# Kernel optimization log

Measured on AMD Instinct MI355X. Metric: run time of the kernel, lower is better.

## Reference

```python
import jax, jax.numpy as jnp
import numpy as np


def setup_inputs() -> dict:
    key = jax.random.key(0)
    k1, k2 = jax.random.split(key)
    B, N, M, D = 4, 8192, 8192, 3
    pred = jax.random.normal(k1, (B, N, D), dtype=jnp.float32)
    target = jax.random.normal(k2, (B, M, D), dtype=jnp.float32)
    return {"pred": pred, "target": target}


def reference(pred, target):
    # Pairwise squared distances via the GEMM cross-term trick:
    # ||p - t||^2 = ||p||^2 + ||t||^2 - 2 <p, t>
    pn = jnp.sum(pred * pred, axis=-1)            # [B, N]
    tn = jnp.sum(target * target, axis=-1)        # [B, M]
    cross = jnp.einsum('bnd,bmd->bnm', pred, target)  # [B, N, M]
    dist = pn[:, :, None] + tn[:, None, :] - 2.0 * cross
    d_pt = jnp.min(dist, axis=2)  # [B, N] pred -> nearest target
    d_tp = jnp.min(dist, axis=1)  # [B, M] target -> nearest pred
    return jnp.mean(d_pt) + jnp.mean(d_tp)
```

## Files before the change

kernel.cpp:

```cpp
#include <hip/hip_runtime.h>
#include <hip/hip_bf16.h>


typedef __attribute__((ext_vector_type(8)))  short short8;
typedef __attribute__((ext_vector_type(16))) float f32x16;

#define BATCH 4
#define NPTS 8192
#define TOTALQ (BATCH * NPTS)
#define BLK 256
#define WNT 2
#define BROWS 256
#define NCH (TOTALQ / BROWS)
#define MSPLIT 8
#define MRANGE (NPTS / MSPLIT)
#define MT_PER (MRANGE / 32)
#define ROW_US 16

#define PACK_US ((size_t)TOTALQ * ROW_US)
#define PART_OFF ((size_t)4 * PACK_US * 2)

__device__ __forceinline__ unsigned short f2bf(float f) {
    unsigned int u = __float_as_uint(f);
    u += 0x7FFFu + ((u >> 16) & 1u);
    return (unsigned short)(u >> 16);
}
__device__ __forceinline__ float bf2f(unsigned short h) {
    return __uint_as_float(((unsigned int)h) << 16);
}
__device__ __forceinline__ unsigned int pk2(unsigned short a, unsigned short b) {
    return (unsigned int)a | ((unsigned int)b << 16);
}

__global__ __launch_bounds__(BLK) void chamfer_pack_kernel(
        const float* __restrict__ pred, const float* __restrict__ target,
        ushort* __restrict__ ws, float* __restrict__ out)
{
    int i = blockIdx.x * BLK + threadIdx.x;
    if (i == 0) out[0] = 0.0f;
    int which = i >> 15;
    int p = i & (TOTALQ - 1);
    const float* src = which ? target : pred;
    float x = src[3 * p], y = src[3 * p + 1], z = src[3 * p + 2];

    unsigned short hx = f2bf(x), hy = f2bf(y), hz = f2bf(z);
    unsigned short lx = f2bf(x - bf2f(hx)), ly = f2bf(y - bf2f(hy)),
                   lz = f2bf(z - bf2f(hz));
    float nrm = fmaf(z, z, fmaf(y, y, x * x));
    unsigned short n1 = f2bf(nrm);
    float r1 = nrm - bf2f(n1);
    unsigned short n2 = f2bf(r1);
    unsigned short n3 = f2bf(r1 - bf2f(n2));
    const unsigned short ONE = 0x3F80;

    unsigned short ax = f2bf(-2.f * bf2f(hx)), ay = f2bf(-2.f * bf2f(hy)),
                   az = f2bf(-2.f * bf2f(hz));
    unsigned short cx = f2bf(-2.f * bf2f(lx)), cy = f2bf(-2.f * bf2f(ly)),
                   cz = f2bf(-2.f * bf2f(lz));

    uint4 A0 = { pk2(ax, ay), pk2(az, cx), pk2(cy, cz), pk2(ax, ay) };
    uint4 A1 = { pk2(az, n1), pk2(n2, n3), pk2(ONE, ONE), pk2(ONE, 0) };
    uint4 B0 = { pk2(hx, hy), pk2(hz, hx), pk2(hy, hz), pk2(lx, ly) };
    uint4 B1 = { pk2(lz, ONE), pk2(ONE, ONE), pk2(n1, n2), pk2(n3, 0) };

    uint4* dA = (uint4*)(ws + (size_t)(2 * which) * PACK_US + (size_t)p * ROW_US);
    uint4* dB = (uint4*)(ws + (size_t)(2 * which + 1) * PACK_US + (size_t)p * ROW_US);
    dA[0] = A0;  dA[1] = A1;
    dB[0] = B0;  dB[1] = B1;
}

__global__ __launch_bounds__(BLK) void chamfer_mfma_kernel(
        const ushort* __restrict__ ws, float* __restrict__ part)
{
    const int dir = blockIdx.z;
    const ushort* packA = ws + (dir ? 2 * PACK_US : 0);
    const ushort* packB = ws + (dir ? 1 * PACK_US : 3 * PACK_US);

    const int nch = blockIdx.x;
    const int b   = nch >> 5;
    const int ms  = blockIdx.y;
    const int w    = threadIdx.x >> 6;
    const int lane = threadIdx.x & 63;
    const int c = lane & 31;
    const int g = lane >> 5;

    __shared__ uint4 ldsb[2][MRANGE];

    {
        const uint4* gB = (const uint4*)(packB +
            ((size_t)b * NPTS + (size_t)ms * MRANGE) * ROW_US);
        #pragma unroll
        for (int r = threadIdx.x; r < MRANGE; r += BLK) {
            ldsb[0][r] = gB[2 * r];
            ldsb[1][r] = gB[2 * r + 1];
        }
    }

    const int rowstart = nch * BROWS + w * (WNT * 32);
    short8 afrag[WNT];
    #pragma unroll
    for (int nt = 0; nt < WNT; ++nt) {
        afrag[nt] = *(const short8*)(
            packA + (size_t)(rowstart + nt * 32 + c) * ROW_US + 8 * g);
    }

    f32x16 acc[WNT];
    #pragma unroll
    for (int nt = 0; nt < WNT; ++nt)
        #pragma unroll
        for (int r = 0; r < 16; ++r)
            acc[nt][r] = 3.4e38f;
    const f32x16 zacc = (f32x16)(0.f);

    __syncthreads();

    const ushort* ldsu = (const ushort*)ldsb;

    #pragma unroll 4
    for (int mt = 0; mt < MT_PER; mt += 2) {
        short8 bf0 = *(const short8*)(ldsu + g * (MRANGE * 8) + (mt * 32 + c) * 8);
        short8 bf1 = *(const short8*)(ldsu + g * (MRANGE * 8) + ((mt + 1) * 32 + c) * 8);
        #pragma unroll
        for (int nt = 0; nt < WNT; ++nt) {
            f32x16 d0 = __builtin_amdgcn_mfma_f32_32x32x16_bf16(
                            afrag[nt], bf0, zacc, 0, 0, 0);
            f32x16 d1 = __builtin_amdgcn_mfma_f32_32x32x16_bf16(
                            afrag[nt], bf1, zacc, 0, 0, 0);
            #pragma unroll
            for (int r = 0; r < 16; ++r)
                acc[nt][r] = fminf(fminf(acc[nt][r], d0[r]), d1[r]);
        }
    }

    float* rp = part + (size_t)(dir * MSPLIT + ms) * TOTALQ + rowstart;
    #pragma unroll
    for (int nt = 0; nt < WNT; ++nt) {
        f32x16 v = acc[nt];
        #pragma unroll
        for (int m = 1; m < 32; m <<= 1) {
            #pragma unroll
            for (int r = 0; r < 16; ++r)
                v[r] = fminf(v[r], __shfl_xor(v[r], m, 64));
        }
        #pragma unroll
        for (int r = 0; r < 16; ++r) {
            int row = (r & 3) + 8 * (r >> 2) + 4 * g;
            if (c == r) rp[nt * 32 + row] = v[r];
        }
    }
}

__global__ __launch_bounds__(BLK) void chamfer_reduce_kernel(
        const float* __restrict__ part, float* __restrict__ out)
{
    int gl = blockIdx.x * BLK + threadIdx.x;
    int dir = gl >> 15, i = gl & (TOTALQ - 1);

    const float* p = part + (size_t)dir * MSPLIT * TOTALQ + i;
    float m = p[0];
    #pragma unroll
    for (int s = 1; s < MSPLIT; ++s)
        m = fminf(m, p[(size_t)s * TOTALQ]);

    float acc = m * (1.0f / (float)TOTALQ);
    #pragma unroll
    for (int off = 32; off > 0; off >>= 1)
        acc += __shfl_down(acc, off, 64);
    __shared__ float wsum[BLK / 64];
    int lane = threadIdx.x & 63, wid = threadIdx.x >> 6;
    if (lane == 0) wsum[wid] = acc;
    __syncthreads();
    if (threadIdx.x == 0) {
        float s = 0.0f;
        #pragma unroll
        for (int wv = 0; wv < BLK / 64; ++wv) s += wsum[wv];
        atomicAdd(out, s);
    }
}

extern "C" void kernel_launch(void* const* d_in, const int* in_sizes, int n_in,
                              void* d_out, int out_size, void* d_ws, size_t ws_size,
                              hipStream_t stream) {
    const float* pred   = (const float*)d_in[0];
    const float* target = (const float*)d_in[1];
    float*       out    = (float*)d_out;
    ushort*      wsp    = (ushort*)d_ws;
    float*       part   = (float*)((char*)d_ws + PART_OFF);

    hipLaunchKernelGGL(chamfer_pack_kernel, dim3(2 * TOTALQ / BLK), dim3(BLK),
                       0, stream, pred, target, wsp, out);

    dim3 grid(NCH, MSPLIT, 2);
    hipLaunchKernelGGL(chamfer_mfma_kernel, grid, dim3(BLK), 0, stream,
                       (const ushort*)wsp, part);

    hipLaunchKernelGGL(chamfer_reduce_kernel, dim3(2 * TOTALQ / BLK), dim3(BLK),
                       0, stream, (const float*)part, out);
}
```

Measured before the change: 95.58 us.

## Fuse point packing into MFMA kernel with staged LDS tiles and single-block reduce

Removes the separate pack kernel: each block now converts its query points and streams target points into LDS in 1024-point stages, splitting them into bf16 hi/lo/norm payloads on the fly. Block rows drop to 128 with one tile per wave and the column split drops to 2, so fewer partial minima are written. The final reduction becomes a single 1024-thread block writing the output directly, with no atomic. The trade-off is redundant per-block recomputation of target payloads, less A-tile reuse per LDS read, and a serial single-block reduce.

```diff
diff --git a/kernel.cpp b/kernel.cpp
--- a/kernel.cpp
+++ b/kernel.cpp
@@ -9,16 +9,13 @@
 #define NPTS 8192
 #define TOTALQ (BATCH * NPTS)
 #define BLK 256
-#define WNT 2
-#define BROWS 256
+#define BROWS 128
 #define NCH (TOTALQ / BROWS)
-#define MSPLIT 8
+#define MSPLIT 2
 #define MRANGE (NPTS / MSPLIT)
-#define MT_PER (MRANGE / 32)
-#define ROW_US 16
-
-#define PACK_US ((size_t)TOTALQ * ROW_US)
-#define PART_OFF ((size_t)4 * PACK_US * 2)
+#define MC 1024
+#define NSTAGE (MRANGE / MC)
+#define MT_PER (MC / 32)
 
 __device__ __forceinline__ unsigned short f2bf(float f) {
     unsigned int u = __float_as_uint(f);
@@ -32,149 +29,135 @@
     return (unsigned int)a | ((unsigned int)b << 16);
 }
 
-__global__ __launch_bounds__(BLK) void chamfer_pack_kernel(
-        const float* __restrict__ pred, const float* __restrict__ target,
-        ushort* __restrict__ ws, float* __restrict__ out)
-{
-    int i = blockIdx.x * BLK + threadIdx.x;
-    if (i == 0) out[0] = 0.0f;
-    int which = i >> 15;
-    int p = i & (TOTALQ - 1);
-    const float* src = which ? target : pred;
-    float x = src[3 * p], y = src[3 * p + 1], z = src[3 * p + 2];
-
-    unsigned short hx = f2bf(x), hy = f2bf(y), hz = f2bf(z);
-    unsigned short lx = f2bf(x - bf2f(hx)), ly = f2bf(y - bf2f(hy)),
-                   lz = f2bf(z - bf2f(hz));
+struct Payload {
+    unsigned short hx, hy, hz, lx, ly, lz, n1, n2, n3;
+};
+__device__ __forceinline__ Payload split_point(float x, float y, float z) {
+    Payload P;
+    P.hx = f2bf(x);  P.hy = f2bf(y);  P.hz = f2bf(z);
+    P.lx = f2bf(x - bf2f(P.hx));
+    P.ly = f2bf(y - bf2f(P.hy));
+    P.lz = f2bf(z - bf2f(P.hz));
     float nrm = fmaf(z, z, fmaf(y, y, x * x));
-    unsigned short n1 = f2bf(nrm);
-    float r1 = nrm - bf2f(n1);
-    unsigned short n2 = f2bf(r1);
-    unsigned short n3 = f2bf(r1 - bf2f(n2));
-    const unsigned short ONE = 0x3F80;
-
-    unsigned short ax = f2bf(-2.f * bf2f(hx)), ay = f2bf(-2.f * bf2f(hy)),
-                   az = f2bf(-2.f * bf2f(hz));
-    unsigned short cx = f2bf(-2.f * bf2f(lx)), cy = f2bf(-2.f * bf2f(ly)),
-                   cz = f2bf(-2.f * bf2f(lz));
-
-    uint4 A0 = { pk2(ax, ay), pk2(az, cx), pk2(cy, cz), pk2(ax, ay) };
-    uint4 A1 = { pk2(az, n1), pk2(n2, n3), pk2(ONE, ONE), pk2(ONE, 0) };
-    uint4 B0 = { pk2(hx, hy), pk2(hz, hx), pk2(hy, hz), pk2(lx, ly) };
-    uint4 B1 = { pk2(lz, ONE), pk2(ONE, ONE), pk2(n1, n2), pk2(n3, 0) };
-
-    uint4* dA = (uint4*)(ws + (size_t)(2 * which) * PACK_US + (size_t)p * ROW_US);
-    uint4* dB = (uint4*)(ws + (size_t)(2 * which + 1) * PACK_US + (size_t)p * ROW_US);
-    dA[0] = A0;  dA[1] = A1;
-    dB[0] = B0;  dB[1] = B1;
+    P.n1 = f2bf(nrm);
+    float r1 = nrm - bf2f(P.n1);
+    P.n2 = f2bf(r1);
+    P.n3 = f2bf(r1 - bf2f(P.n2));
+    return P;
 }
 
-__global__ __launch_bounds__(BLK) void chamfer_mfma_kernel(
-        const ushort* __restrict__ ws, float* __restrict__ part)
+__global__ __launch_bounds__(BLK) void chamfer_mega_kernel(
+        const float* __restrict__ pred, const float* __restrict__ target,
+        float* __restrict__ part)
 {
     const int dir = blockIdx.z;
-    const ushort* packA = ws + (dir ? 2 * PACK_US : 0);
-    const ushort* packB = ws + (dir ? 1 * PACK_US : 3 * PACK_US);
+    const float* __restrict__ Q  = dir ? target : pred;
+    const float* __restrict__ Tg = dir ? pred : target;
 
     const int nch = blockIdx.x;
-    const int b   = nch >> 5;
+    const int b   = nch >> 6;
     const int ms  = blockIdx.y;
     const int w    = threadIdx.x >> 6;
     const int lane = threadIdx.x & 63;
     const int c = lane & 31;
     const int g = lane >> 5;
+    const unsigned short ONE = 0x3F80;
 
-    __shared__ uint4 ldsb[2][MRANGE];
+    __shared__ uint4 ldsb[2][MC];
 
+    const int rowstart = nch * BROWS + w * 32;
+    short8 afrag;
     {
-        const uint4* gB = (const uint4*)(packB +
-            ((size_t)b * NPTS + (size_t)ms * MRANGE) * ROW_US);
+        int r = rowstart + c;
+        float x = Q[3 * r], y = Q[3 * r + 1], z = Q[3 * r + 2];
+        Payload P = split_point(x, y, z);
+        unsigned short ax = f2bf(-2.f * bf2f(P.hx)),
+                       ay = f2bf(-2.f * bf2f(P.hy)),
+                       az = f2bf(-2.f * bf2f(P.hz));
+        unsigned short cx = f2bf(-2.f * bf2f(P.lx)),
+                       cy = f2bf(-2.f * bf2f(P.ly)),
+                       cz = f2bf(-2.f * bf2f(P.lz));
+        uint4 h0 = { pk2(ax, ay), pk2(az, cx), pk2(cy, cz), pk2(ax, ay) };
+        uint4 h1 = { pk2(az, P.n1), pk2(P.n2, P.n3), pk2(ONE, ONE), pk2(ONE, 0) };
+        uint4 sel = g ? h1 : h0;
+        afrag = *(short8*)&sel;
+    }
+
+    f32x16 acc;
+    #pragma unroll
+    for (int r = 0; r < 16; ++r) acc[r] = 3.4e38f;
+    const f32x16 zacc = (f32x16)(0.f);
+
+    const size_t colbase = (size_t)b * NPTS + (size_t)ms * MRANGE;
+
+    for (int st = 0; st < NSTAGE; ++st) {
+        __syncthreads();
         #pragma unroll
-        for (int r = threadIdx.x; r < MRANGE; r += BLK) {
-            ldsb[0][r] = gB[2 * r];
-            ldsb[1][r] = gB[2 * r + 1];
+        for (int j = 0; j < MC / BLK; ++j) {
+            int p = j * BLK + threadIdx.x;
+            size_t gp = colbase + st * MC + p;
+            float x = Tg[3 * gp], y = Tg[3 * gp + 1], z = Tg[3 * gp + 2];
+            Payload P = split_point(x, y, z);
+            ldsb[0][p] = (uint4){ pk2(P.hx, P.hy), pk2(P.hz, P.hx),
+                                  pk2(P.hy, P.hz), pk2(P.lx, P.ly) };
+            ldsb[1][p] = (uint4){ pk2(P.lz, ONE), pk2(ONE, ONE),
+                                  pk2(P.n1, P.n2), pk2(P.n3, 0) };
+        }
+        __syncthreads();
+
+        const ushort* ldsu = (const ushort*)&ldsb[g][0];
+        #pragma unroll 2
+        for (int mt = 0; mt < MT_PER; mt += 2) {
+            short8 bf0 = *(const short8*)(ldsu + (mt * 32 + c) * 8);
+            short8 bf1 = *(const short8*)(ldsu + ((mt + 1) * 32 + c) * 8);
+            f32x16 d0 = __builtin_amdgcn_mfma_f32_32x32x16_bf16(
+                            afrag, bf0, zacc, 0, 0, 0);
+            f32x16 d1 = __builtin_amdgcn_mfma_f32_32x32x16_bf16(
+                            afrag, bf1, zacc, 0, 0, 0);
+            #pragma unroll
+            for (int r = 0; r < 16; ++r)
+                acc[r] = fminf(fminf(acc[r], d0[r]), d1[r]);
         }
     }
 
-    const int rowstart = nch * BROWS + w * (WNT * 32);
-    short8 afrag[WNT];
     #pragma unroll
-    for (int nt = 0; nt < WNT; ++nt) {
-        afrag[nt] = *(const short8*)(
-            packA + (size_t)(rowstart + nt * 32 + c) * ROW_US + 8 * g);
-    }
-
-    f32x16 acc[WNT];
-    #pragma unroll
-    for (int nt = 0; nt < WNT; ++nt)
+    for (int m = 1; m < 32; m <<= 1) {
         #pragma unroll
         for (int r = 0; r < 16; ++r)
-            acc[nt][r] = 3.4e38f;
-    const f32x16 zacc = (f32x16)(0.f);
-
-    __syncthreads();
-
-    const ushort* ldsu = (const ushort*)ldsb;
-
-    #pragma unroll 4
-    for (int mt = 0; mt < MT_PER; mt += 2) {
-        short8 bf0 = *(const short8*)(ldsu + g * (MRANGE * 8) + (mt * 32 + c) * 8);
-        short8 bf1 = *(const short8*)(ldsu + g * (MRANGE * 8) + ((mt + 1) * 32 + c) * 8);
-        #pragma unroll
-        for (int nt = 0; nt < WNT; ++nt) {
-            f32x16 d0 = __builtin_amdgcn_mfma_f32_32x32x16_bf16(
-                            afrag[nt], bf0, zacc, 0, 0, 0);
-            f32x16 d1 = __builtin_amdgcn_mfma_f32_32x32x16_bf16(
-                            afrag[nt], bf1, zacc, 0, 0, 0);
-            #pragma unroll
-            for (int r = 0; r < 16; ++r)
-                acc[nt][r] = fminf(fminf(acc[nt][r], d0[r]), d1[r]);
-        }
+            acc[r] = fminf(acc[r], __shfl_xor(acc[r], m, 64));
     }
-
     float* rp = part + (size_t)(dir * MSPLIT + ms) * TOTALQ + rowstart;
     #pragma unroll
-    for (int nt = 0; nt < WNT; ++nt) {
-        f32x16 v = acc[nt];
-        #pragma unroll
-        for (int m = 1; m < 32; m <<= 1) {
-            #pragma unroll
-            for (int r = 0; r < 16; ++r)
-                v[r] = fminf(v[r], __shfl_xor(v[r], m, 64));
-        }
-        #pragma unroll
-        for (int r = 0; r < 16; ++r) {
-            int row = (r & 3) + 8 * (r >> 2) + 4 * g;
-            if (c == r) rp[nt * 32 + row] = v[r];
-        }
+    for (int r = 0; r < 16; ++r) {
+        int row = (r & 3) + 8 * (r >> 2) + 4 * g;
+        if (c == r) rp[row] = acc[r];
     }
 }
 
-__global__ __launch_bounds__(BLK) void chamfer_reduce_kernel(
+__global__ __launch_bounds__(1024) void chamfer_reduce_kernel(
         const float* __restrict__ part, float* __restrict__ out)
 {
-    int gl = blockIdx.x * BLK + threadIdx.x;
-    int dir = gl >> 15, i = gl & (TOTALQ - 1);
-
-    const float* p = part + (size_t)dir * MSPLIT * TOTALQ + i;
-    float m = p[0];
+    float acc = 0.0f;
     #pragma unroll
-    for (int s = 1; s < MSPLIT; ++s)
-        m = fminf(m, p[(size_t)s * TOTALQ]);
-
-    float acc = m * (1.0f / (float)TOTALQ);
+    for (int dir = 0; dir < 2; ++dir) {
+        const float* p0 = part + (size_t)(dir * MSPLIT) * TOTALQ;
+        const float* p1 = p0 + TOTALQ;
+        for (int i = threadIdx.x; i < TOTALQ; i += 1024)
+            acc += fminf(p0[i], p1[i]);
+    }
+    acc *= (1.0f / (float)TOTALQ);
     #pragma unroll
     for (int off = 32; off > 0; off >>= 1)
         acc += __shfl_down(acc, off, 64);
-    __shared__ float wsum[BLK / 64];
+    __shared__ float wsum[16];
     int lane = threadIdx.x & 63, wid = threadIdx.x >> 6;
     if (lane == 0) wsum[wid] = acc;
     __syncthreads();
     if (threadIdx.x == 0) {
         float s = 0.0f;
         #pragma unroll
-        for (int wv = 0; wv < BLK / 64; ++wv) s += wsum[wv];
-        atomicAdd(out, s);
+        for (int wv = 0; wv < 16; ++wv) s += wsum[wv];
+        out[0] = s;
     }
 }
 
@@ -184,16 +167,12 @@
     const float* pred   = (const float*)d_in[0];
     const float* target = (const float*)d_in[1];
     float*       out    = (float*)d_out;
-    ushort*      wsp    = (ushort*)d_ws;
-    float*       part   = (float*)((char*)d_ws + PART_OFF);
-
-    hipLaunchKernelGGL(chamfer_pack_kernel, dim3(2 * TOTALQ / BLK), dim3(BLK),
-                       0, stream, pred, target, wsp, out);
+    float*       part   = (float*)d_ws;
 
     dim3 grid(NCH, MSPLIT, 2);
-    hipLaunchKernelGGL(chamfer_mfma_kernel, grid, dim3(BLK), 0, stream,
-                       (const ushort*)wsp, part);
+    hipLaunchKernelGGL(chamfer_mega_kernel, grid, dim3(BLK), 0, stream,
+                       pred, target, part);
 
-    hipLaunchKernelGGL(chamfer_reduce_kernel, dim3(2 * TOTALQ / BLK), dim3(BLK),
-                       0, stream, (const float*)part, out);
+    hipLaunchKernelGGL(chamfer_reduce_kernel, dim3(1), dim3(1024), 0, stream,
+                       (const float*)part, out);
 }
```

Measured after the change: 105.9 us. 1.11x slower.
